# Performance work log

Hardware: AMD Instinct MI355X
Metric: run time of the kernel (lower is better)

## Reference

```python
import jax, jax.numpy as jnp
import numpy as np


def setup_inputs() -> dict:
    key = jax.random.key(0)
    k1, k2, k3, k4 = jax.random.split(key, 4)
    B, S, E, H = 8, 2048, 1024, 64
    x = jax.random.normal(k1, (B, S, E), dtype=jnp.float32)
    # nn.Linear(E, H, bias=False) weight is (H, E); we store transposed (E, H)
    scale = 1.0 / np.sqrt(E)
    Wk = jax.random.normal(k2, (E, H), dtype=jnp.float32) * scale
    Wq = jax.random.normal(k3, (E, H), dtype=jnp.float32) * scale
    Wv = jax.random.normal(k4, (E, H), dtype=jnp.float32) * scale
    return {"x": x, "Wk": Wk, "Wq": Wq, "Wv": Wv}


def reference(x, Wk, Wq, Wv):
    # x: (B, S, E); projections: (B, S, H)
    k = x @ Wk
    q = x @ Wq
    v = x @ Wv
    H = k.shape[-1]
    # scores: (B, S, S) with 1/sqrt(H) scaling as in the torch code
    scores = jnp.einsum("bqh,bkh->bqk", q, k) * (H ** -0.5)
    S = x.shape[1]
    causal = jnp.triu(jnp.full((S, S), -jnp.inf, dtype=scores.dtype), k=1)
    wei = jax.nn.softmax(scores + causal, axis=-1)
    # dropout p=0.0 -> identity
    return jnp.einsum("bqk,bkh->bqh", wei, v)
```

## Files before the change

### kernel.cpp

```cpp
#include <hip/hip_runtime.h>
#include <hip/hip_bf16.h>

typedef unsigned short ushort_t;
typedef __attribute__((ext_vector_type(8))) short short8;
typedef __attribute__((ext_vector_type(4))) short short4v;
typedef __attribute__((ext_vector_type(4))) float f32x4;

__device__ __forceinline__ float bf2f(ushort_t u) {
    unsigned int x = ((unsigned int)u) << 16;
    float f; __builtin_memcpy(&f, &x, 4); return f;
}
__device__ __forceinline__ ushort_t f2bf(float f) {
    __hip_bfloat16 h = __float2bfloat16(f);
    ushort_t u; __builtin_memcpy(&u, &h, 2); return u;
}
__device__ __forceinline__ unsigned packbf2(float a, float b) {
    return (unsigned)f2bf(a) | ((unsigned)f2bf(b) << 16);
}

constexpr int E  = 1024;
constexpr int Hd = 64;
constexpr int S  = 2048;
constexpr int ROWS = 8 * 2048;
constexpr int NTOT = 192;
constexpr int LST  = 88;
constexpr int LSTA = 72;

__global__ __launch_bounds__(256)
void prep_wt(const float* __restrict__ Wk, const float* __restrict__ Wq,
             const float* __restrict__ Wv, ushort_t* __restrict__ WT)
{
    int idx = blockIdx.x * 256 + threadIdx.x;
    int n = idx >> 10;
    int kk = idx & 1023;
    const float* W = (n < 64) ? Wq : ((n < 128) ? Wk : Wv);
    int h = n & 63;
    WT[idx] = f2bf(W[kk * Hd + h]);
}

__global__ __launch_bounds__(256)
void proj_v7(const float* __restrict__ x, const ushort_t* __restrict__ WT,
             ushort_t* __restrict__ qo, ushort_t* __restrict__ ko,
             ushort_t* __restrict__ vTo)
{
    __shared__ alignas(16) ushort_t XS0[32][LST];
    __shared__ alignas(16) ushort_t XS1[32][LST];

    const int t    = threadIdx.x;
    const int w    = t >> 6;
    const int lane = t & 63;
    const int m    = lane & 15;
    const int g    = lane >> 4;
    const int rb   = blockIdx.x * 32;

    f32x4 accq[2], acck[2], accv[2];
    #pragma unroll
    for (int j = 0; j < 2; ++j) {
        accq[j] = (f32x4){0.f, 0.f, 0.f, 0.f};
        acck[j] = (f32x4){0.f, 0.f, 0.f, 0.f};
        accv[j] = (f32x4){0.f, 0.f, 0.f, 0.f};
    }

    const float* xptr = x + (size_t)(rb + (t >> 3)) * E + (t & 7) * 8;
    const ushort_t* wqp = WT + (size_t)(w * 16 + m) * E + g * 8;
    const ushort_t* wkp = wqp + (size_t)64 * E;
    const ushort_t* wvp = wqp + (size_t)128 * E;

    const int sr = t >> 3, sc = (t & 7) * 8;

    float4 xA0 = *(const float4*)xptr;
    float4 xA1 = *(const float4*)(xptr + 4);
    float4 xB0 = *(const float4*)(xptr + 64);
    float4 xB1 = *(const float4*)(xptr + 64 + 4);

    short8 wAq[2], wAk[2], wAv[2], wBq[2], wBk[2], wBv[2];
    #pragma unroll
    for (int kt = 0; kt < 2; ++kt) {
        wAq[kt] = *(const short8*)(wqp + kt * 32);
        wAk[kt] = *(const short8*)(wkp + kt * 32);
        wAv[kt] = *(const short8*)(wvp + kt * 32);
    }

    #pragma unroll 1
    for (int cc = 0; cc < 16; cc += 2) {
        {
            uint4 sv;
            sv.x = packbf2(xA0.x, xA0.y);
            sv.y = packbf2(xA0.z, xA0.w);
            sv.z = packbf2(xA1.x, xA1.y);
            sv.w = packbf2(xA1.z, xA1.w);
            *(uint4*)&XS0[sr][sc] = sv;
        }
        __syncthreads();
        if (cc + 2 < 16) {
            const int k0 = (cc + 2) * 64;
            xA0 = *(const float4*)(xptr + k0);
            xA1 = *(const float4*)(xptr + k0 + 4);
        }
        {
            const int k0 = (cc + 1) * 64;
            #pragma unroll
            for (int kt = 0; kt < 2; ++kt) {
                wBq[kt] = *(const short8*)(wqp + k0 + kt * 32);
                wBk[kt] = *(const short8*)(wkp + k0 + kt * 32);
                wBv[kt] = *(const short8*)(wvp + k0 + kt * 32);
            }
        }
        #pragma unroll
        for (int kt = 0; kt < 2; ++kt) {
            short8 a0 = *(const short8*)&XS0[m][kt * 32 + g * 8];
            short8 a1 = *(const short8*)&XS0[16 + m][kt * 32 + g * 8];
            accq[0] = __builtin_amdgcn_mfma_f32_16x16x32_bf16(a0, wAq[kt], accq[0], 0, 0, 0);
            accq[1] = __builtin_amdgcn_mfma_f32_16x16x32_bf16(a1, wAq[kt], accq[1], 0, 0, 0);
            acck[0] = __builtin_amdgcn_mfma_f32_16x16x32_bf16(a0, wAk[kt], acck[0], 0, 0, 0);
            acck[1] = __builtin_amdgcn_mfma_f32_16x16x32_bf16(a1, wAk[kt], acck[1], 0, 0, 0);
            accv[0] = __builtin_amdgcn_mfma_f32_16x16x32_bf16(wAv[kt], a0, accv[0], 0, 0, 0);
            accv[1] = __builtin_amdgcn_mfma_f32_16x16x32_bf16(wAv[kt], a1, accv[1], 0, 0, 0);
        }

        {
            uint4 sv;
            sv.x = packbf2(xB0.x, xB0.y);
            sv.y = packbf2(xB0.z, xB0.w);
            sv.z = packbf2(xB1.x, xB1.y);
            sv.w = packbf2(xB1.z, xB1.w);
            *(uint4*)&XS1[sr][sc] = sv;
        }
        __syncthreads();
        if (cc + 3 < 16) {
            const int k0 = (cc + 3) * 64;
            xB0 = *(const float4*)(xptr + k0);
            xB1 = *(const float4*)(xptr + k0 + 4);
        }
        if (cc + 2 < 16) {
            const int k0 = (cc + 2) * 64;
            #pragma unroll
            for (int kt = 0; kt < 2; ++kt) {
                wAq[kt] = *(const short8*)(wqp + k0 + kt * 32);
                wAk[kt] = *(const short8*)(wkp + k0 + kt * 32);
                wAv[kt] = *(const short8*)(wvp + k0 + kt * 32);
            }
        }
        #pragma unroll
        for (int kt = 0; kt < 2; ++kt) {
            short8 a0 = *(const short8*)&XS1[m][kt * 32 + g * 8];
            short8 a1 = *(const short8*)&XS1[16 + m][kt * 32 + g * 8];
            accq[0] = __builtin_amdgcn_mfma_f32_16x16x32_bf16(a0, wBq[kt], accq[0], 0, 0, 0);
            accq[1] = __builtin_amdgcn_mfma_f32_16x16x32_bf16(a1, wBq[kt], accq[1], 0, 0, 0);
            acck[0] = __builtin_amdgcn_mfma_f32_16x16x32_bf16(a0, wBk[kt], acck[0], 0, 0, 0);
            acck[1] = __builtin_amdgcn_mfma_f32_16x16x32_bf16(a1, wBk[kt], acck[1], 0, 0, 0);
            accv[0] = __builtin_amdgcn_mfma_f32_16x16x32_bf16(wBv[kt], a0, accv[0], 0, 0, 0);
            accv[1] = __builtin_amdgcn_mfma_f32_16x16x32_bf16(wBv[kt], a1, accv[1], 0, 0, 0);
        }
    }

    const int col   = w * 16 + m;
    const int batch = rb >> 11;
    const int seq0  = rb & (S - 1);
    #pragma unroll
    for (int mt = 0; mt < 2; ++mt) {
        const int orow = rb + mt * 16 + g * 4;
        #pragma unroll
        for (int r = 0; r < 4; ++r) {
            qo[(size_t)(orow + r) * Hd + col] = f2bf(accq[mt][r] * 0.125f);
            ko[(size_t)(orow + r) * Hd + col] = f2bf(acck[mt][r]);
        }
    }
    #pragma unroll
    for (int ns = 0; ns < 2; ++ns)
        #pragma unroll
        for (int r = 0; r < 4; ++r) {
            const int h = w * 16 + g * 4 + r;
            vTo[(size_t)batch * Hd * S + (size_t)h * S + seq0 + ns * 16 + m]
                = f2bf(accv[ns][r]);
        }
}

__global__ __launch_bounds__(256)
void attn_part(const ushort_t* __restrict__ q, const ushort_t* __restrict__ k,
               const ushort_t* __restrict__ vT,
               float* __restrict__ lp, ushort_t* __restrict__ op)
{
    const int bi     = blockIdx.x;
    const int parity = bi & 3;
    const int pr     = bi >> 2;
    const int batch  = pr & 7;
    const int tile   = 31 - (pr >> 3);
    const int qs0    = tile * 64;
    const int sidx   = (batch * 32 + tile) * 4 + parity;

    const ushort_t* kb  = k  + (size_t)batch * S * Hd;
    const ushort_t* vTb = vT + (size_t)batch * Hd * S;

    const int t    = threadIdx.x;
    const int w    = t >> 6;
    const int lane = t & 63;
    const int m    = lane & 15;
    const int g    = lane >> 4;

    __shared__ alignas(16) ushort_t KS [2][64][LSTA];
    __shared__ alignas(16) ushort_t VTS[2][64][LSTA];

    const ushort_t* qrow = q + (size_t)(batch * S + qs0 + w * 16 + m) * Hd;
    short8 qf0 = *(const short8*)(qrow + g * 8);
    short8 qf1 = *(const short8*)(qrow + 32 + g * 8);

    f32x4 o[4];
    #pragma unroll
    for (int j = 0; j < 4; ++j) o[j] = (f32x4){0.f, 0.f, 0.f, 0.f};
    float lrun = 0.f;
    const int qr = w * 16 + m;

    const int r1 = t >> 3, c16 = (t & 7) * 8;
    uint4 pk0, pk1, pv0, pv1;

    int c = parity;
    if (c <= tile) {
        const int key0 = c * 64;
        const ushort_t* kt_base = kb + (size_t)key0 * Hd;
        pk0 = *(const uint4*)(kt_base + t * 8);
        pk1 = *(const uint4*)(kt_base + (t + 256) * 8);
        pv0 = *(const uint4*)(vTb + (size_t)r1 * S + key0 + c16);
        pv1 = *(const uint4*)(vTb + (size_t)(r1 + 32) * S + key0 + c16);
    }

    int bit = 0;
    for (; c <= tile; c += 4, bit ^= 1) {
        *(uint4*)&KS [bit][r1][c16]       = pk0;
        *(uint4*)&KS [bit][r1 + 32][c16]  = pk1;
        *(uint4*)&VTS[bit][r1][c16]       = pv0;
        *(uint4*)&VTS[bit][r1 + 32][c16]  = pv1;
        __syncthreads();

        if (c + 4 <= tile) {
            const int key0n = (c + 4) * 64;
            const ushort_t* kt_base = kb + (size_t)key0n * Hd;
            pk0 = *(const uint4*)(kt_base + t * 8);
            pk1 = *(const uint4*)(kt_base + (t + 256) * 8);
            pv0 = *(const uint4*)(vTb + (size_t)r1 * S + key0n + c16);
            pv1 = *(const uint4*)(vTb + (size_t)(r1 + 32) * S + key0n + c16);
        }

        f32x4 sacc[4];
        #pragma unroll
        for (int j = 0; j < 4; ++j) sacc[j] = (f32x4){0.f, 0.f, 0.f, 0.f};
        #pragma unroll
        for (int nt = 0; nt < 4; ++nt) {
            short8 b0 = *(const short8*)&KS[bit][nt * 16 + m][g * 8];
            short8 b1 = *(const short8*)&KS[bit][nt * 16 + m][32 + g * 8];
            sacc[nt] = __builtin_amdgcn_mfma_f32_16x16x32_bf16(b0, qf0, sacc[nt], 0, 0, 0);
            sacc[nt] = __builtin_amdgcn_mfma_f32_16x16x32_bf16(b1, qf1, sacc[nt], 0, 0, 0);
        }

        if (c == tile) {
            #pragma unroll
            for (int nt = 0; nt < 4; ++nt)
                #pragma unroll
                for (int r = 0; r < 4; ++r) {
                    const int keyl = nt * 16 + g * 4 + r;
                    sacc[nt][r] = (keyl > qr) ? 0.f : __expf(sacc[nt][r]);
                }
        } else {
            #pragma unroll
            for (int nt = 0; nt < 4; ++nt)
                #pragma unroll
                for (int r = 0; r < 4; ++r)
                    sacc[nt][r] = __expf(sacc[nt][r]);
        }

        #pragma unroll
        for (int nt = 0; nt < 4; ++nt)
            lrun += (sacc[nt][0] + sacc[nt][1]) + (sacc[nt][2] + sacc[nt][3]);

        unsigned pw0[4], pw1[4];
        #pragma unroll
        for (int s = 0; s < 4; ++s) {
            pw0[s] = packbf2(sacc[s][0], sacc[s][1]);
            pw1[s] = packbf2(sacc[s][2], sacc[s][3]);
        }

        #pragma unroll
        for (int s = 0; s < 4; ++s) {
            short4v pa;
            { unsigned u2[2] = {pw0[s], pw1[s]}; __builtin_memcpy(&pa, u2, 8); }
            #pragma unroll
            for (int nt = 0; nt < 4; ++nt) {
                short4v vb = *(const short4v*)&VTS[bit][nt * 16 + m][s * 16 + g * 4];
                o[nt] = __builtin_amdgcn_mfma_f32_16x16x16bf16_1k(pa, vb, o[nt], 0, 0, 0);
            }
        }
    }

    {
        float ts = lrun;
        ts += __shfl_xor(ts, 16, 64);
        ts += __shfl_xor(ts, 32, 64);
        if (lane < 16) lp[sidx * 64 + w * 16 + m] = ts;
    }
    #pragma unroll
    for (int nt = 0; nt < 4; ++nt)
        #pragma unroll
        for (int r = 0; r < 4; ++r)
            op[(size_t)sidx * 4096 + (w * 16 + g * 4 + r) * 64 + nt * 16 + m]
                = f2bf(o[nt][r]);
}

__global__ __launch_bounds__(256)
void attn_merge(const float* __restrict__ lp, const ushort_t* __restrict__ op,
                float* __restrict__ out)
{
    const int bq    = blockIdx.x;
    const int batch = bq >> 5;
    const int tile  = bq & 31;
    const int s0    = (batch * 32 + tile) * 4;

    const int t   = threadIdx.x;
    const int row = t >> 2;
    const int c16 = (t & 3) * 16;

    float l = 0.f;
    #pragma unroll
    for (int p = 0; p < 4; ++p) l += lp[(s0 + p) * 64 + row];
    const float inv = 1.f / l;

    float acc[16];
    #pragma unroll
    for (int j = 0; j < 16; ++j) acc[j] = 0.f;
    #pragma unroll
    for (int p = 0; p < 4; ++p) {
        short8 a0 = *(const short8*)(op + (size_t)(s0 + p) * 4096 + row * 64 + c16);
        short8 a1 = *(const short8*)(op + (size_t)(s0 + p) * 4096 + row * 64 + c16 + 8);
        #pragma unroll
        for (int j = 0; j < 8; ++j) {
            acc[j]     += bf2f((ushort_t)a0[j]);
            acc[j + 8] += bf2f((ushort_t)a1[j]);
        }
    }
    float* dst = out + (size_t)(batch * S + tile * 64 + row) * Hd + c16;
    #pragma unroll
    for (int j = 0; j < 16; ++j) dst[j] = acc[j] * inv;
}

extern "C" void kernel_launch(void* const* d_in, const int* in_sizes, int n_in,
                              void* d_out, int out_size, void* d_ws, size_t ws_size,
                              hipStream_t stream) {
    const float* x  = (const float*)d_in[0];
    const float* Wk = (const float*)d_in[1];
    const float* Wq = (const float*)d_in[2];
    const float* Wv = (const float*)d_in[3];
    float* out = (float*)d_out;

    ushort_t* qws  = (ushort_t*)d_ws;
    ushort_t* kws  = qws + (size_t)ROWS * Hd;
    ushort_t* vTws = kws + (size_t)ROWS * Hd;
    ushort_t* WT   = vTws + (size_t)ROWS * Hd;
    float*    lpp  = (float*)(WT + (size_t)NTOT * E);
    ushort_t* opp  = (ushort_t*)(lpp + 1024 * 64);

    prep_wt<<<(NTOT * E) / 256, 256, 0, stream>>>(Wk, Wq, Wv, WT);
    proj_v7<<<ROWS / 32, 256, 0, stream>>>(x, WT, qws, kws, vTws);
    attn_part<<<1024, 256, 0, stream>>>(qws, kws, vTws, lpp, opp);
    attn_merge<<<256, 256, 0, stream>>>(lpp, opp, out);
}
```

Baseline: 135.0 us.

## Load K and V fragments directly from global memory, drop LDS staging

The attention kernel no longer stages K and V^T tiles through double-buffered shared memory with a block barrier. Each wave now loads its own MFMA operand fragments straight from global memory (relying on L1/L2 for reuse across the four waves). Block-index decoding is also reordered so batch varies fastest, which changes which blocks run together and how work spreads over the device. This removes LDS traffic and __syncthreads, but each wave now issues redundant global loads and loses the explicit software prefetch of the next tile.

```diff
diff --git a/kernel.cpp b/kernel.cpp
--- a/kernel.cpp
+++ b/kernel.cpp
@@ -24,7 +24,6 @@
 constexpr int ROWS = 8 * 2048;
 constexpr int NTOT = 192;
 constexpr int LST  = 88;
-constexpr int LSTA = 72;
 
 __global__ __launch_bounds__(256)
 void prep_wt(const float* __restrict__ Wk, const float* __restrict__ Wq,
@@ -182,10 +181,10 @@
                float* __restrict__ lp, ushort_t* __restrict__ op)
 {
     const int bi     = blockIdx.x;
-    const int parity = bi & 3;
-    const int pr     = bi >> 2;
-    const int batch  = pr & 7;
-    const int tile   = 31 - (pr >> 3);
+    const int batch  = bi & 7;
+    const int u      = bi >> 3;
+    const int parity = u & 3;
+    const int tile   = 31 - (u >> 2);
     const int qs0    = tile * 64;
     const int sidx   = (batch * 32 + tile) * 4 + parity;
 
@@ -198,9 +197,6 @@
     const int m    = lane & 15;
     const int g    = lane >> 4;
 
-    __shared__ alignas(16) ushort_t KS [2][64][LSTA];
-    __shared__ alignas(16) ushort_t VTS[2][64][LSTA];
-
     const ushort_t* qrow = q + (size_t)(batch * S + qs0 + w * 16 + m) * Hd;
     short8 qf0 = *(const short8*)(qrow + g * 8);
     short8 qf1 = *(const short8*)(qrow + 32 + g * 8);
@@ -211,34 +207,27 @@
     float lrun = 0.f;
     const int qr = w * 16 + m;
 
-    const int r1 = t >> 3, c16 = (t & 7) * 8;
-    uint4 pk0, pk1, pv0, pv1;
-
-    int c = parity;
-    if (c <= tile) {
+    const ushort_t* kAddr = kb  + (size_t)m * Hd + g * 8;
+    const ushort_t* vAddr = vTb + (size_t)m * S  + g * 4;
+
+    #pragma unroll 1
+    for (int c = parity; c <= tile; c += 4) {
         const int key0 = c * 64;
-        const ushort_t* kt_base = kb + (size_t)key0 * Hd;
-        pk0 = *(const uint4*)(kt_base + t * 8);
-        pk1 = *(const uint4*)(kt_base + (t + 256) * 8);
-        pv0 = *(const uint4*)(vTb + (size_t)r1 * S + key0 + c16);
-        pv1 = *(const uint4*)(vTb + (size_t)(r1 + 32) * S + key0 + c16);
-    }
-
-    int bit = 0;
-    for (; c <= tile; c += 4, bit ^= 1) {
-        *(uint4*)&KS [bit][r1][c16]       = pk0;
-        *(uint4*)&KS [bit][r1 + 32][c16]  = pk1;
-        *(uint4*)&VTS[bit][r1][c16]       = pv0;
-        *(uint4*)&VTS[bit][r1 + 32][c16]  = pv1;
-        __syncthreads();
-
-        if (c + 4 <= tile) {
-            const int key0n = (c + 4) * 64;
-            const ushort_t* kt_base = kb + (size_t)key0n * Hd;
-            pk0 = *(const uint4*)(kt_base + t * 8);
-            pk1 = *(const uint4*)(kt_base + (t + 256) * 8);
-            pv0 = *(const uint4*)(vTb + (size_t)r1 * S + key0n + c16);
-            pv1 = *(const uint4*)(vTb + (size_t)(r1 + 32) * S + key0n + c16);
+
+        short8 kf[4][2];
+        #pragma unroll
+        for (int nt = 0; nt < 4; ++nt) {
+            const ushort_t* p = kAddr + (size_t)(key0 + nt * 16) * Hd;
+            kf[nt][0] = *(const short8*)p;
+            kf[nt][1] = *(const short8*)(p + 32);
+        }
+        short4v vf[4][4];
+        #pragma unroll
+        for (int nt = 0; nt < 4; ++nt) {
+            const ushort_t* p = vAddr + (size_t)(nt * 16) * S + key0;
+            #pragma unroll
+            for (int s = 0; s < 4; ++s)
+                vf[nt][s] = *(const short4v*)(p + s * 16);
         }
 
         f32x4 sacc[4];
@@ -246,10 +235,8 @@
         for (int j = 0; j < 4; ++j) sacc[j] = (f32x4){0.f, 0.f, 0.f, 0.f};
         #pragma unroll
         for (int nt = 0; nt < 4; ++nt) {
-            short8 b0 = *(const short8*)&KS[bit][nt * 16 + m][g * 8];
-            short8 b1 = *(const short8*)&KS[bit][nt * 16 + m][32 + g * 8];
-            sacc[nt] = __builtin_amdgcn_mfma_f32_16x16x32_bf16(b0, qf0, sacc[nt], 0, 0, 0);
-            sacc[nt] = __builtin_amdgcn_mfma_f32_16x16x32_bf16(b1, qf1, sacc[nt], 0, 0, 0);
+            sacc[nt] = __builtin_amdgcn_mfma_f32_16x16x32_bf16(kf[nt][0], qf0, sacc[nt], 0, 0, 0);
+            sacc[nt] = __builtin_amdgcn_mfma_f32_16x16x32_bf16(kf[nt][1], qf1, sacc[nt], 0, 0, 0);
         }
 
         if (c == tile) {
@@ -284,10 +271,8 @@
             short4v pa;
             { unsigned u2[2] = {pw0[s], pw1[s]}; __builtin_memcpy(&pa, u2, 8); }
             #pragma unroll
-            for (int nt = 0; nt < 4; ++nt) {
-                short4v vb = *(const short4v*)&VTS[bit][nt * 16 + m][s * 16 + g * 4];
-                o[nt] = __builtin_amdgcn_mfma_f32_16x16x16bf16_1k(pa, vb, o[nt], 0, 0, 0);
-            }
+            for (int nt = 0; nt < 4; ++nt)
+                o[nt] = __builtin_amdgcn_mfma_f32_16x16x16bf16_1k(pa, vf[nt][s], o[nt], 0, 0, 0);
         }
     }
 
```

Measured after the change: 180.1 us. 1.33x slower.
